# Performance work log

Measured on AMD Instinct MI355X. Metric: run time of the kernel, lower is better.

Reference implementation:

```python
import jax, jax.numpy as jnp
import numpy as np

B = 16384
QD = 2048   # query_dim
KD = 1024   # key_dim
HID = 1024  # hidden_dim = min(QD, KD)
NH = 16     # num_heads
HD = HID // NH  # head_dim = 64
LN_EPS = 1e-5


def _ln(x, w, b):
    m = jnp.mean(x, axis=-1, keepdims=True)
    v = jnp.mean((x - m) ** 2, axis=-1, keepdims=True)
    return (x - m) * jax.lax.rsqrt(v + LN_EPS) * w + b


def _lin(x, W, b):
    return x @ W.T + b


def setup_inputs() -> dict:
    key = jax.random.key(0)
    ks = jax.random.split(key, 12)
    p = lambda k, shape: jax.random.normal(k, shape, jnp.float32) * 0.02
    return dict(
        query_features=jax.random.normal(ks[0], (B, QD), jnp.float32),
        key_features=jax.random.normal(ks[1], (B, KD), jnp.float32),
        Wq=p(ks[2], (HID, QD)), bq=jnp.zeros((HID,), jnp.float32),
        ln_q_w=jnp.ones((HID,), jnp.float32), ln_q_b=jnp.zeros((HID,), jnp.float32),
        Wk=p(ks[3], (HID, KD)), bk=jnp.zeros((HID,), jnp.float32),
        ln_k_w=jnp.ones((HID,), jnp.float32), ln_k_b=jnp.zeros((HID,), jnp.float32),
        Wvq=p(ks[4], (HID, QD)), bvq=jnp.zeros((HID,), jnp.float32),
        Wvk=p(ks[5], (HID, KD)), bvk=jnp.zeros((HID,), jnp.float32),
        Wo=p(ks[6], (QD, HID)), bo=jnp.zeros((QD,), jnp.float32),
        ln_o_w=jnp.ones((QD,), jnp.float32), ln_o_b=jnp.zeros((QD,), jnp.float32),
        Wg1=p(ks[7], (HID, QD + KD)), bg1=jnp.zeros((HID,), jnp.float32),
        Wg2=p(ks[8], (1, HID)), bg2=jnp.zeros((1,), jnp.float32),
        Wc1=p(ks[9], (HID, QD + KD)), bc1=jnp.zeros((HID,), jnp.float32),
        Wc2=p(ks[10], (1, HID)), bc2=jnp.zeros((1,), jnp.float32),
    )


def reference(query_features, key_features,
              Wq, bq, ln_q_w, ln_q_b,
              Wk, bk, ln_k_w, ln_k_b,
              Wvq, bvq, Wvk, bvk,
              Wo, bo, ln_o_w, ln_o_b,
              Wg1, bg1, Wg2, bg2,
              Wc1, bc1, Wc2, bc2):
    b = query_features.shape[0]
    q = _ln(_lin(query_features, Wq, bq), ln_q_w, ln_q_b)      # [B, HID]
    k = _ln(_lin(key_features, Wk, bk), ln_k_w, ln_k_b)        # [B, HID]
    v_q = _lin(query_features, Wvq, bvq)  # computed in torch but unused
    v_k = _lin(key_features, Wvk, bvk)    # [B, HID]
    q = q.reshape(b, NH, HD)
    k = k.reshape(b, NH, HD)
    v_k = v_k.reshape(b, NH, HD)
    # NOTE: attention mixes over the HEAD axis (j == num_heads), per original einsum
    scores = jnp.einsum('bhd,bjd->bhj', q, k) / np.sqrt(HD).astype(np.float32)
    attn = jax.nn.softmax(scores, axis=-1)  # dropout p effectively 0 / eval mode
    attended = jnp.einsum('bhj,bjd->bhd', attn, v_k).reshape(b, HID)
    output = _ln(_lin(attended, Wo, bo), ln_o_w, ln_o_b)       # [B, QD]
    combined = jnp.concatenate([query_features, key_features], axis=1)  # [B, QD+KD]
    gate = jax.nn.sigmoid(_lin(jax.nn.gelu(_lin(combined, Wg1, bg1), approximate=False), Wg2, bg2))
    chem = jax.nn.sigmoid(_lin(jax.nn.gelu(_lin(combined, Wc1, bc1), approximate=False), Wc2, bc2))
    effective_gate = gate * chem  # [B, 1]
    return query_features + effective_gate * output
```

## Files before the change

kernel.cpp:

```cpp
#include <hip/hip_runtime.h>
#include <stdint.h>

#define QD 2048
#define KD 1024
#define HID 1024
#define NH 16
#define HD 64
#define CMBD 3072

typedef float  f32x4   __attribute__((ext_vector_type(4)));
typedef short  short8  __attribute__((ext_vector_type(8)));
typedef short  short4v __attribute__((ext_vector_type(4)));
typedef float  float4v __attribute__((ext_vector_type(4)));

__device__ inline float bf2f(short s) {
  unsigned u = ((unsigned)(unsigned short)s) << 16;
  return __builtin_bit_cast(float, u);
}
__device__ inline short f2bf(float f) {
  unsigned u = __builtin_bit_cast(unsigned, f);
  u = u + 0x7fff + ((u >> 16) & 1);
  return (short)(u >> 16);
}

__global__ void cvt_bf16(const float* __restrict__ s, short* __restrict__ d) {
  size_t i = ((size_t)blockIdx.x * blockDim.x + threadIdx.x) * 4;
  float4v v = *(const float4v*)(s + i);
  short4v o;
  o[0] = f2bf(v[0]); o[1] = f2bf(v[1]); o[2] = f2bf(v[2]); o[3] = f2bf(v[3]);
  *(short4v*)(d + i) = o;
}

__global__ void cvt_concat(const float* __restrict__ s, short* __restrict__ d,
                           int ncols4, int ldd) {
  int i = blockIdx.x * blockDim.x + threadIdx.x;
  int row = i / ncols4;
  int c4  = i - row * ncols4;
  float4v v = *(const float4v*)(s + (size_t)row * (ncols4 * 4) + c4 * 4);
  short4v o;
  o[0] = f2bf(v[0]); o[1] = f2bf(v[1]); o[2] = f2bf(v[2]); o[3] = f2bf(v[3]);
  *(short4v*)(d + (size_t)row * ldd + c4 * 4) = o;
}

#define EPI_NONE 0
#define EPI_GELU 1

typedef const __attribute__((address_space(1))) void gvoid_t;
typedef __attribute__((address_space(3))) void lvoid_t;

#define WAIT_VM(n)  asm volatile("s_waitcnt vmcnt(" #n ")" ::: "memory")
#define WAIT_LGKM0  asm volatile("s_waitcnt lgkmcnt(0)" ::: "memory")

template<int EPI>
__global__ __launch_bounds__(512, 2)
void gemm256(const short* __restrict__ A, size_t lda,
             const short* __restrict__ W,
             const float* __restrict__ bias,
             short* __restrict__ C, int N, int K) {
  extern __shared__ short ls[];
  const int tid  = threadIdx.x;
  const int lane = tid & 63;
  const int wave = tid >> 6;
  const int wm = wave >> 2, wn = wave & 3;
  const int fr = lane & 15, kq4 = lane >> 4;

  const int nwg = gridDim.x * gridDim.y;
  const int lin = blockIdx.y * gridDim.x + blockIdx.x;
  const int cpx = nwg >> 3;
  const int nid = (lin & 7) * cpx + (lin >> 3);
  const int bx = nid % gridDim.x, by = nid / gridDim.x;
  const size_t rowBase = (size_t)by * 256;
  const size_t colBase = (size_t)bx * 256;

  const int NT = K >> 5;

  f32x4 acc[8][4];
#pragma unroll
  for (int mi = 0; mi < 8; mi++)
#pragma unroll
    for (int ni = 0; ni < 4; ni++) acc[mi][ni] = (f32x4){0.f, 0.f, 0.f, 0.f};

  const int frsw = (kq4 ^ ((fr >> 1) & 3)) * 8;
  const int aoff = (wm * 128 + fr) * 32 + frsw;
  const int boff = 8192 + (wn * 64 + fr) * 32 + frsw;

  const int grow  = tid >> 2;
  const int slotx = (tid & 3) ^ ((tid >> 3) & 3);
  const short* pA0 = A + (rowBase + grow) * lda + slotx * 8;
  const short* pA1 = pA0 + (size_t)128 * lda;
  const short* pB0 = W + (colBase + grow) * (size_t)K + slotx * 8;
  const short* pB1 = pB0 + (size_t)128 * K;
  short* const dst0 = ls + tid * 8;

  auto STAGE = [&](int slot) {
    short* d = dst0 + slot * 16384;
    __builtin_amdgcn_global_load_lds((gvoid_t*)pA0, (lvoid_t*)d,            16, 0, 0);
    __builtin_amdgcn_global_load_lds((gvoid_t*)pA1, (lvoid_t*)(d + 4096),   16, 0, 0);
    __builtin_amdgcn_global_load_lds((gvoid_t*)pB0, (lvoid_t*)(d + 8192),   16, 0, 0);
    __builtin_amdgcn_global_load_lds((gvoid_t*)pB1, (lvoid_t*)(d + 12288),  16, 0, 0);
    pA0 += 32; pA1 += 32; pB0 += 32; pB1 += 32;
  };

  STAGE(0); STAGE(1); STAGE(2);
  WAIT_VM(8);
  __builtin_amdgcn_s_barrier();

  for (int t = 0; t < NT; ++t) {
    const short* sl = ls + (t & 3) * 16384;
    if (t + 3 < NT) STAGE((t + 3) & 3);

    short8 af[8], bf[4];
#pragma unroll
    for (int m = 0; m < 8; m++) af[m] = *(const short8*)(sl + aoff + m * 512);
#pragma unroll
    for (int n = 0; n < 4; n++) bf[n] = *(const short8*)(sl + boff + n * 512);

    __builtin_amdgcn_s_setprio(1);
#pragma unroll
    for (int m = 0; m < 8; m++)
#pragma unroll
      for (int n = 0; n < 4; n++)
        acc[m][n] = __builtin_amdgcn_mfma_f32_16x16x32_bf16(af[m], bf[n], acc[m][n], 0, 0, 0);
    __builtin_amdgcn_s_setprio(0);

    WAIT_LGKM0;
    const int rem = NT - 2 - t;
    if (rem >= 2)      { WAIT_VM(8); }
    else if (rem == 1) { WAIT_VM(4); }
    else               { WAIT_VM(0); }
    __builtin_amdgcn_s_barrier();
  }

#pragma unroll
  for (int mi = 0; mi < 8; mi++) {
    const size_t row0 = rowBase + wm * 128 + mi * 16 + kq4 * 4;
#pragma unroll
    for (int ni = 0; ni < 4; ni++) {
      const int col = (int)colBase + wn * 64 + ni * 16 + fr;
      const float bv = bias[col];
#pragma unroll
      for (int j = 0; j < 4; j++) {
        float x = acc[mi][ni][j] + bv;
        if (EPI == EPI_GELU) x = 0.5f * x * (1.f + erff(x * 0.70710678118f));
        C[(row0 + j) * (size_t)N + col] = f2bf(x);
      }
    }
  }
}

__device__ inline float2 block_sum2(float a, float b, float* sc) {
#pragma unroll
  for (int o = 32; o >= 1; o >>= 1) {
    a += __shfl_down(a, o);
    b += __shfl_down(b, o);
  }
  const int lane = threadIdx.x & 63, w = threadIdx.x >> 6;
  const int nw = blockDim.x >> 6;
  if (lane == 0) { sc[w * 2] = a; sc[w * 2 + 1] = b; }
  __syncthreads();
  float ra = 0.f, rb = 0.f;
  for (int i = 0; i < nw; i++) { ra += sc[i * 2]; rb += sc[i * 2 + 1]; }
  __syncthreads();
  return make_float2(ra, rb);
}

__global__ __launch_bounds__(256)
void attn_ln(const short* __restrict__ qp, const short* __restrict__ kv,
             const float* __restrict__ lnqw, const float* __restrict__ lnqb,
             const float* __restrict__ lnkw, const float* __restrict__ lnkb,
             short* __restrict__ att) {
  __shared__ float qs[HID];
  __shared__ float ks[NH * 65];
  __shared__ float vs[HID];
  __shared__ float aw[256];
  __shared__ float red[8];
  const int t = threadIdx.x;
  const size_t row = blockIdx.x;

  short4v q4 = *(const short4v*)(qp + row * HID + t * 4);
  short4v k4 = *(const short4v*)(kv + row * 2048 + t * 4);
  short4v v4 = *(const short4v*)(kv + row * 2048 + 1024 + t * 4);
  float qv[4], kvv[4];
  float sq = 0.f, sqq = 0.f, sk = 0.f, skk = 0.f;
#pragma unroll
  for (int i = 0; i < 4; i++) {
    qv[i] = bf2f(q4[i]); sq += qv[i]; sqq += qv[i] * qv[i];
    kvv[i] = bf2f(k4[i]); sk += kvv[i]; skk += kvv[i] * kvv[i];
  }
  float2 rq = block_sum2(sq, sqq, red);
  float mq = rq.x / HID, vq = rq.y / HID - mq * mq;
  float rsq = rsqrtf(vq + 1e-5f);
  float2 rk = block_sum2(sk, skk, red);
  float mk = rk.x / HID, vv = rk.y / HID - mk * mk;
  float rsk = rsqrtf(vv + 1e-5f);
#pragma unroll
  for (int i = 0; i < 4; i++) {
    const int idx = t * 4 + i;
    qs[idx] = (qv[i] - mq) * rsq * lnqw[idx] + lnqb[idx];
    ks[(idx >> 6) * 65 + (idx & 63)] = (kvv[i] - mk) * rsk * lnkw[idx] + lnkb[idx];
    vs[idx] = bf2f(v4[i]);
  }
  __syncthreads();

  const int h = t >> 4, j = t & 15;
  float s = 0.f;
#pragma unroll 8
  for (int d = 0; d < 64; d++) s += qs[h * 64 + d] * ks[j * 65 + d];
  s *= 0.125f;
  float mx = s;
#pragma unroll
  for (int o = 8; o >= 1; o >>= 1) mx = fmaxf(mx, __shfl_xor(mx, o, 16));
  float e = __expf(s - mx);
  float sum = e;
#pragma unroll
  for (int o = 8; o >= 1; o >>= 1) sum += __shfl_xor(sum, o, 16);
  aw[t] = e / sum;
  __syncthreads();

  const int dB = (t & 15) * 4;
  float o0 = 0.f, o1 = 0.f, o2 = 0.f, o3 = 0.f;
#pragma unroll
  for (int jj = 0; jj < 16; jj++) {
    const float w = aw[h * 16 + jj];
    const float* vp = &vs[jj * 64 + dB];
    o0 += w * vp[0]; o1 += w * vp[1]; o2 += w * vp[2]; o3 += w * vp[3];
  }
  short4v o4;
  o4[0] = f2bf(o0); o4[1] = f2bf(o1); o4[2] = f2bf(o2); o4[3] = f2bf(o3);
  *(short4v*)(att + row * HID + h * 64 + dB) = o4;
}

__global__ __launch_bounds__(256)
void gate_kernel(const short* __restrict__ hgc,
                 const float* __restrict__ wg2, const float* __restrict__ bg2,
                 const float* __restrict__ wc2, const float* __restrict__ bc2,
                 float* __restrict__ eg) {
  __shared__ float red[8];
  const int t = threadIdx.x;
  const size_t row = blockIdx.x;
  short4v g4 = *(const short4v*)(hgc + row * 2048 + t * 4);
  short4v c4 = *(const short4v*)(hgc + row * 2048 + 1024 + t * 4);
  float sg = 0.f, sc = 0.f;
#pragma unroll
  for (int i = 0; i < 4; i++) {
    sg += bf2f(g4[i]) * wg2[t * 4 + i];
    sc += bf2f(c4[i]) * wc2[t * 4 + i];
  }
  float2 r = block_sum2(sg, sc, red);
  if (t == 0) {
    float g = 1.f / (1.f + __expf(-(r.x + bg2[0])));
    float c = 1.f / (1.f + __expf(-(r.y + bc2[0])));
    eg[row] = g * c;
  }
}

__global__ __launch_bounds__(256)
void final_kernel(const short* __restrict__ opre, const float* __restrict__ qf,
                  const float* __restrict__ eg,
                  const float* __restrict__ lnow, const float* __restrict__ lnob,
                  float* __restrict__ out) {
  __shared__ float red[8];
  const int t = threadIdx.x;
  const size_t row = blockIdx.x;
  short8 o8 = *(const short8*)(opre + row * QD + t * 8);
  float x[8];
  float s = 0.f, ss = 0.f;
#pragma unroll
  for (int i = 0; i < 8; i++) { x[i] = bf2f(o8[i]); s += x[i]; ss += x[i] * x[i]; }
  float2 r = block_sum2(s, ss, red);
  float m = r.x / QD, v = r.y / QD - m * m;
  float rs = rsqrtf(v + 1e-5f);
  float g = eg[row];
  float4v oa, ob;
#pragma unroll
  for (int i = 0; i < 8; i++) {
    const int c = t * 8 + i;
    float y = (x[i] - m) * rs * lnow[c] + lnob[c];
    float r2 = qf[row * QD + c] + g * y;
    if (i < 4) oa[i] = r2; else ob[i - 4] = r2;
  }
  *(float4v*)(out + row * QD + t * 8) = oa;
  *(float4v*)(out + row * QD + t * 8 + 4) = ob;
}

extern "C" void kernel_launch(void* const* d_in, const int* in_sizes, int n_in,
                              void* d_out, int out_size, void* d_ws, size_t ws_size,
                              hipStream_t stream) {
  const float* qf   = (const float*)d_in[0];
  const float* kf   = (const float*)d_in[1];
  const float* Wq   = (const float*)d_in[2];
  const float* bq   = (const float*)d_in[3];
  const float* lnqw = (const float*)d_in[4];
  const float* lnqb = (const float*)d_in[5];
  const float* Wk   = (const float*)d_in[6];
  const float* bk   = (const float*)d_in[7];
  const float* lnkw = (const float*)d_in[8];
  const float* lnkb = (const float*)d_in[9];
  const float* Wvk  = (const float*)d_in[12];
  const float* bvk  = (const float*)d_in[13];
  const float* Wo   = (const float*)d_in[14];
  const float* bo   = (const float*)d_in[15];
  const float* lnow = (const float*)d_in[16];
  const float* lnob = (const float*)d_in[17];
  const float* Wg1  = (const float*)d_in[18];
  const float* bg1  = (const float*)d_in[19];
  const float* Wg2  = (const float*)d_in[20];
  const float* bg2  = (const float*)d_in[21];
  const float* Wc1  = (const float*)d_in[22];
  const float* bc1  = (const float*)d_in[23];
  const float* Wc2  = (const float*)d_in[24];
  const float* bc2  = (const float*)d_in[25];

  const int rows = in_sizes[0] / QD;

  char* ws = (char*)d_ws;
  size_t off = 0;
  auto alloc = [&](size_t bytes) -> char* {
    char* p = ws + off;
    off += (bytes + 255) & ~(size_t)255;
    return p;
  };
  short* cmb  = (short*)alloc((size_t)rows * CMBD * 2);
  short* wqb  = (short*)alloc((size_t)HID * QD * 2);
  short* wkv  = (short*)alloc((size_t)2 * HID * KD * 2);
  short* wob  = (short*)alloc((size_t)QD * HID * 2);
  short* wgc  = (short*)alloc((size_t)2 * HID * CMBD * 2);
  short* hgc  = (short*)alloc((size_t)rows * 2048 * 2);
  short* qp   = (short*)alloc((size_t)rows * HID * 2);
  short* kvp  = (short*)alloc((size_t)rows * 2048 * 2);
  float* eg   = (float*)alloc((size_t)rows * 4);
  float* bgc  = (float*)alloc(2048 * 4);
  float* bkv  = (float*)alloc(2048 * 4);
  short* att  = hgc;
  short* opre = cmb;

  hipMemcpyAsync(bgc, bg1, HID * 4, hipMemcpyDeviceToDevice, stream);
  hipMemcpyAsync(bgc + HID, bc1, HID * 4, hipMemcpyDeviceToDevice, stream);
  hipMemcpyAsync(bkv, bk, HID * 4, hipMemcpyDeviceToDevice, stream);
  hipMemcpyAsync(bkv + HID, bvk, HID * 4, hipMemcpyDeviceToDevice, stream);

  cvt_concat<<<rows * 2, 256, 0, stream>>>(qf, cmb, QD / 4, CMBD);
  cvt_concat<<<rows, 256, 0, stream>>>(kf, cmb + QD, KD / 4, CMBD);
  cvt_bf16<<<(HID * QD / 4) / 256, 256, 0, stream>>>(Wq, wqb);
  cvt_bf16<<<(HID * KD / 4) / 256, 256, 0, stream>>>(Wk, wkv);
  cvt_bf16<<<(HID * KD / 4) / 256, 256, 0, stream>>>(Wvk, wkv + (size_t)HID * KD);
  cvt_bf16<<<(QD * HID / 4) / 256, 256, 0, stream>>>(Wo, wob);
  cvt_bf16<<<(HID * CMBD / 4) / 256, 256, 0, stream>>>(Wg1, wgc);
  cvt_bf16<<<(HID * CMBD / 4) / 256, 256, 0, stream>>>(Wc1, wgc + (size_t)HID * CMBD);

  hipFuncSetAttribute((const void*)gemm256<EPI_GELU>,
                      hipFuncAttributeMaxDynamicSharedMemorySize, 131072);
  hipFuncSetAttribute((const void*)gemm256<EPI_NONE>,
                      hipFuncAttributeMaxDynamicSharedMemorySize, 131072);

  const dim3 blk(512);
  const int mt = rows / 256;
  const size_t lds = 131072;

  gemm256<EPI_GELU><<<dim3(2048 / 256, mt), blk, lds, stream>>>(cmb, CMBD, wgc, bgc, hgc, 2048, CMBD);
  gate_kernel<<<rows, 256, 0, stream>>>(hgc, Wg2, bg2, Wc2, bc2, eg);
  gemm256<EPI_NONE><<<dim3(1024 / 256, mt), blk, lds, stream>>>(cmb, CMBD, wqb, bq, qp, 1024, QD);
  gemm256<EPI_NONE><<<dim3(2048 / 256, mt), blk, lds, stream>>>(cmb + QD, CMBD, wkv, bkv, kvp, 2048, KD);
  attn_ln<<<rows, 256, 0, stream>>>(qp, kvp, lnqw, lnqb, lnkw, lnkb, att);
  gemm256<EPI_NONE><<<dim3(2048 / 256, mt), blk, lds, stream>>>(att, HID, wob, bo, opre, 2048, HID);
  final_kernel<<<rows, 256, 0, stream>>>(opre, qf, eg, lnow, lnob, (float*)d_out);
}
```

Before: 656.0 us.

## Load GEMM weight fragments straight to registers and shrink LDS staging to three A buffers

The GEMM kernel no longer stages the weight (B) tile through LDS. Each wave loads its own B fragments from global memory into double-buffered registers, and only the A tile goes through a 3-slot LDS ring held in a static 48KB shared array. This removes LDS traffic and capacity pressure for B, which may allow more blocks per CU. In exchange, B fragments are fetched per wave with less coalescing and are reloaded redundantly by waves sharing a column, and the loop now needs two barriers per iteration.

```diff
diff --git a/kernel.cpp b/kernel.cpp
--- a/kernel.cpp
+++ b/kernel.cpp
@@ -49,7 +49,6 @@
 typedef __attribute__((address_space(3))) void lvoid_t;
 
 #define WAIT_VM(n)  asm volatile("s_waitcnt vmcnt(" #n ")" ::: "memory")
-#define WAIT_LGKM0  asm volatile("s_waitcnt lgkmcnt(0)" ::: "memory")
 
 template<int EPI>
 __global__ __launch_bounds__(512, 2)
@@ -57,7 +56,7 @@
              const short* __restrict__ W,
              const float* __restrict__ bias,
              short* __restrict__ C, int N, int K) {
-  extern __shared__ short ls[];
+  __shared__ short ls[3 * 8192];
   const int tid  = threadIdx.x;
   const int lane = tid & 63;
   const int wave = tid >> 6;
@@ -82,54 +81,62 @@
 
   const int frsw = (kq4 ^ ((fr >> 1) & 3)) * 8;
   const int aoff = (wm * 128 + fr) * 32 + frsw;
-  const int boff = 8192 + (wn * 64 + fr) * 32 + frsw;
 
   const int grow  = tid >> 2;
   const int slotx = (tid & 3) ^ ((tid >> 3) & 3);
   const short* pA0 = A + (rowBase + grow) * lda + slotx * 8;
   const short* pA1 = pA0 + (size_t)128 * lda;
-  const short* pB0 = W + (colBase + grow) * (size_t)K + slotx * 8;
-  const short* pB1 = pB0 + (size_t)128 * K;
   short* const dst0 = ls + tid * 8;
 
   auto STAGE = [&](int slot) {
-    short* d = dst0 + slot * 16384;
-    __builtin_amdgcn_global_load_lds((gvoid_t*)pA0, (lvoid_t*)d,            16, 0, 0);
-    __builtin_amdgcn_global_load_lds((gvoid_t*)pA1, (lvoid_t*)(d + 4096),   16, 0, 0);
-    __builtin_amdgcn_global_load_lds((gvoid_t*)pB0, (lvoid_t*)(d + 8192),   16, 0, 0);
-    __builtin_amdgcn_global_load_lds((gvoid_t*)pB1, (lvoid_t*)(d + 12288),  16, 0, 0);
-    pA0 += 32; pA1 += 32; pB0 += 32; pB1 += 32;
+    short* d = dst0 + slot * 8192;
+    __builtin_amdgcn_global_load_lds((gvoid_t*)pA0, (lvoid_t*)d,          16, 0, 0);
+    __builtin_amdgcn_global_load_lds((gvoid_t*)pA1, (lvoid_t*)(d + 4096), 16, 0, 0);
+    pA0 += 32; pA1 += 32;
   };
 
-  STAGE(0); STAGE(1); STAGE(2);
-  WAIT_VM(8);
-  __builtin_amdgcn_s_barrier();
-
-  for (int t = 0; t < NT; ++t) {
-    const short* sl = ls + (t & 3) * 16384;
-    if (t + 3 < NT) STAGE((t + 3) & 3);
-
-    short8 af[8], bf[4];
-#pragma unroll
-    for (int m = 0; m < 8; m++) af[m] = *(const short8*)(sl + aoff + m * 512);
-#pragma unroll
-    for (int n = 0; n < 4; n++) bf[n] = *(const short8*)(sl + boff + n * 512);
-
-    __builtin_amdgcn_s_setprio(1);
-#pragma unroll
-    for (int m = 0; m < 8; m++)
-#pragma unroll
-      for (int n = 0; n < 4; n++)
-        acc[m][n] = __builtin_amdgcn_mfma_f32_16x16x32_bf16(af[m], bf[n], acc[m][n], 0, 0, 0);
-    __builtin_amdgcn_s_setprio(0);
-
-    WAIT_LGKM0;
-    const int rem = NT - 2 - t;
-    if (rem >= 2)      { WAIT_VM(8); }
-    else if (rem == 1) { WAIT_VM(4); }
-    else               { WAIT_VM(0); }
-    __builtin_amdgcn_s_barrier();
-  }
+  const short* pb = W + (colBase + wn * 64 + fr) * (size_t)K + kq4 * 8;
+  short8 bE[4], bO[4];
+
+  STAGE(0);
+#pragma unroll
+  for (int n = 0; n < 4; n++) bE[n] = *(const short8*)(pb + n * 16 * (size_t)K);
+  pb += 32;
+  STAGE(1);
+
+#define GITER(T, bC, bN)                                                      \
+  {                                                                           \
+    const int t_ = (T);                                                       \
+    if (t_ + 1 < NT) {                                                        \
+      _Pragma("unroll")                                                       \
+      for (int n = 0; n < 4; n++)                                             \
+        bN[n] = *(const short8*)(pb + n * 16 * (size_t)K);                    \
+      pb += 32;                                                               \
+    }                                                                         \
+    if (t_ + 2 < NT) STAGE((t_ + 2) % 3);                                     \
+    if (t_ + 2 < NT)       { WAIT_VM(12); }                                   \
+    else if (t_ + 2 == NT) { WAIT_VM(10); }                                   \
+    else                   { WAIT_VM(4); }                                    \
+    __builtin_amdgcn_s_barrier();                                             \
+    const short* sl_ = ls + (t_ % 3) * 8192;                                  \
+    short8 af_[8];                                                            \
+    _Pragma("unroll")                                                         \
+    for (int m = 0; m < 8; m++) af_[m] = *(const short8*)(sl_ + aoff + m * 512); \
+    __builtin_amdgcn_s_setprio(1);                                            \
+    _Pragma("unroll")                                                         \
+    for (int m = 0; m < 8; m++)                                               \
+      _Pragma("unroll")                                                       \
+      for (int n = 0; n < 4; n++)                                             \
+        acc[m][n] = __builtin_amdgcn_mfma_f32_16x16x32_bf16(af_[m], bC[n], acc[m][n], 0, 0, 0); \
+    __builtin_amdgcn_s_setprio(0);                                            \
+    __builtin_amdgcn_s_barrier();                                             \
+  }
+
+  for (int t = 0; t < NT; t += 2) {
+    GITER(t,     bE, bO)
+    GITER(t + 1, bO, bE)
+  }
+#undef GITER
 
 #pragma unroll
   for (int mi = 0; mi < 8; mi++) {
@@ -348,20 +355,14 @@
   cvt_bf16<<<(HID * CMBD / 4) / 256, 256, 0, stream>>>(Wg1, wgc);
   cvt_bf16<<<(HID * CMBD / 4) / 256, 256, 0, stream>>>(Wc1, wgc + (size_t)HID * CMBD);
 
-  hipFuncSetAttribute((const void*)gemm256<EPI_GELU>,
-                      hipFuncAttributeMaxDynamicSharedMemorySize, 131072);
-  hipFuncSetAttribute((const void*)gemm256<EPI_NONE>,
-                      hipFuncAttributeMaxDynamicSharedMemorySize, 131072);
-
   const dim3 blk(512);
   const int mt = rows / 256;
-  const size_t lds = 131072;
-
-  gemm256<EPI_GELU><<<dim3(2048 / 256, mt), blk, lds, stream>>>(cmb, CMBD, wgc, bgc, hgc, 2048, CMBD);
+
+  gemm256<EPI_GELU><<<dim3(2048 / 256, mt), blk, 0, stream>>>(cmb, CMBD, wgc, bgc, hgc, 2048, CMBD);
   gate_kernel<<<rows, 256, 0, stream>>>(hgc, Wg2, bg2, Wc2, bc2, eg);
-  gemm256<EPI_NONE><<<dim3(1024 / 256, mt), blk, lds, stream>>>(cmb, CMBD, wqb, bq, qp, 1024, QD);
-  gemm256<EPI_NONE><<<dim3(2048 / 256, mt), blk, lds, stream>>>(cmb + QD, CMBD, wkv, bkv, kvp, 2048, KD);
+  gemm256<EPI_NONE><<<dim3(1024 / 256, mt), blk, 0, stream>>>(cmb, CMBD, wqb, bq, qp, 1024, QD);
+  gemm256<EPI_NONE><<<dim3(2048 / 256, mt), blk, 0, stream>>>(cmb + QD, CMBD, wkv, bkv, kvp, 2048, KD);
   attn_ln<<<rows, 256, 0, stream>>>(qp, kvp, lnqw, lnqb, lnkw, lnkb, att);
-  gemm256<EPI_NONE><<<dim3(2048 / 256, mt), blk, lds, stream>>>(att, HID, wob, bo, opre, 2048, HID);
+  gemm256<EPI_NONE><<<dim3(2048 / 256, mt), blk, 0, stream>>>(att, HID, wob, bo, opre, 2048, HID);
   final_kernel<<<rows, 256, 0, stream>>>(opre, qf, eg, lnow, lnob, (float*)d_out);
 }
```

Measured after the change: 886.9 us. 35.2% more time.

## Fuse gate second layer into GEMM epilogue and retile GEMM to four waves

Applied to the files above, without the earlier changes.

The gate/chem second linear layer (GELU then dot with Wg2/Wc2) now runs in the first GEMM's epilogue, with per-row partial sums accumulated by atomicAdd. This removes the hidden-activation store, the separate gate kernel and its re-read. The sigmoid product moves into the final kernel. The GEMM also changes from 512 threads with 4-deep dynamic LDS buffering to 256 threads, each wave holding a 128x128 accumulator, with 3-deep static LDS buffering. This raises register pressure and lowers wave count per CU, and the atomics make the gate sums nondeterministic. The attention LN reductions are merged into a single block reduction.

```diff
diff --git a/kernel.cpp b/kernel.cpp
--- a/kernel.cpp
+++ b/kernel.cpp
@@ -44,24 +44,27 @@
 
 #define EPI_NONE 0
 #define EPI_GELU 1
+#define EPI_GATE 2
 
 typedef const __attribute__((address_space(1))) void gvoid_t;
 typedef __attribute__((address_space(3))) void lvoid_t;
 
 #define WAIT_VM(n)  asm volatile("s_waitcnt vmcnt(" #n ")" ::: "memory")
-#define WAIT_LGKM0  asm volatile("s_waitcnt lgkmcnt(0)" ::: "memory")
+
+#define SLOT 16384
 
 template<int EPI>
-__global__ __launch_bounds__(512, 2)
+__global__ __launch_bounds__(256, 1)
 void gemm256(const short* __restrict__ A, size_t lda,
              const short* __restrict__ W,
              const float* __restrict__ bias,
-             short* __restrict__ C, int N, int K) {
-  extern __shared__ short ls[];
+             short* __restrict__ C, int N, int K,
+             const float* __restrict__ w2, float* __restrict__ egp, int rowsTot) {
+  __shared__ short ls[3 * SLOT];
   const int tid  = threadIdx.x;
   const int lane = tid & 63;
   const int wave = tid >> 6;
-  const int wm = wave >> 2, wn = wave & 3;
+  const int wm = wave >> 1, wn = wave & 1;
   const int fr = lane & 15, kq4 = lane >> 4;
 
   const int nwg = gridDim.x * gridDim.y;
@@ -74,92 +77,134 @@
 
   const int NT = K >> 5;
 
-  f32x4 acc[8][4];
+  f32x4 acc[8][8];
 #pragma unroll
   for (int mi = 0; mi < 8; mi++)
 #pragma unroll
-    for (int ni = 0; ni < 4; ni++) acc[mi][ni] = (f32x4){0.f, 0.f, 0.f, 0.f};
+    for (int ni = 0; ni < 8; ni++) acc[mi][ni] = (f32x4){0.f, 0.f, 0.f, 0.f};
 
   const int frsw = (kq4 ^ ((fr >> 1) & 3)) * 8;
   const int aoff = (wm * 128 + fr) * 32 + frsw;
-  const int boff = 8192 + (wn * 64 + fr) * 32 + frsw;
+  const int boff = 8192 + (wn * 128 + fr) * 32 + frsw;
 
   const int grow  = tid >> 2;
   const int slotx = (tid & 3) ^ ((tid >> 3) & 3);
-  const short* pA0 = A + (rowBase + grow) * lda + slotx * 8;
-  const short* pA1 = pA0 + (size_t)128 * lda;
-  const short* pB0 = W + (colBase + grow) * (size_t)K + slotx * 8;
-  const short* pB1 = pB0 + (size_t)128 * K;
+  const short* pA = A + (rowBase + grow) * lda + slotx * 8;
+  const short* pB = W + (colBase + grow) * (size_t)K + slotx * 8;
+  const size_t stepA = 64 * lda, stepB = 64 * (size_t)K;
   short* const dst0 = ls + tid * 8;
 
   auto STAGE = [&](int slot) {
-    short* d = dst0 + slot * 16384;
-    __builtin_amdgcn_global_load_lds((gvoid_t*)pA0, (lvoid_t*)d,            16, 0, 0);
-    __builtin_amdgcn_global_load_lds((gvoid_t*)pA1, (lvoid_t*)(d + 4096),   16, 0, 0);
-    __builtin_amdgcn_global_load_lds((gvoid_t*)pB0, (lvoid_t*)(d + 8192),   16, 0, 0);
-    __builtin_amdgcn_global_load_lds((gvoid_t*)pB1, (lvoid_t*)(d + 12288),  16, 0, 0);
-    pA0 += 32; pA1 += 32; pB0 += 32; pB1 += 32;
+    short* d = dst0 + slot * SLOT;
+#pragma unroll
+    for (int p = 0; p < 4; p++)
+      __builtin_amdgcn_global_load_lds((gvoid_t*)(pA + p * stepA),
+          (lvoid_t*)(d + p * 2048), 16, 0, 0);
+#pragma unroll
+    for (int p = 0; p < 4; p++)
+      __builtin_amdgcn_global_load_lds((gvoid_t*)(pB + p * stepB),
+          (lvoid_t*)(d + 8192 + p * 2048), 16, 0, 0);
+    pA += 32; pB += 32;
   };
 
-  STAGE(0); STAGE(1); STAGE(2);
+  STAGE(0); STAGE(1);
   WAIT_VM(8);
   __builtin_amdgcn_s_barrier();
 
   for (int t = 0; t < NT; ++t) {
-    const short* sl = ls + (t & 3) * 16384;
-    if (t + 3 < NT) STAGE((t + 3) & 3);
-
-    short8 af[8], bf[4];
+    if (t + 2 < NT) STAGE((t + 2) % 3);
+    const short* sl = ls + (t % 3) * SLOT;
+    short8 af[8], bf[8];
 #pragma unroll
     for (int m = 0; m < 8; m++) af[m] = *(const short8*)(sl + aoff + m * 512);
 #pragma unroll
-    for (int n = 0; n < 4; n++) bf[n] = *(const short8*)(sl + boff + n * 512);
+    for (int n = 0; n < 8; n++) bf[n] = *(const short8*)(sl + boff + n * 512);
 
     __builtin_amdgcn_s_setprio(1);
 #pragma unroll
     for (int m = 0; m < 8; m++)
 #pragma unroll
-      for (int n = 0; n < 4; n++)
+      for (int n = 0; n < 8; n++)
         acc[m][n] = __builtin_amdgcn_mfma_f32_16x16x32_bf16(af[m], bf[n], acc[m][n], 0, 0, 0);
     __builtin_amdgcn_s_setprio(0);
 
-    WAIT_LGKM0;
-    const int rem = NT - 2 - t;
-    if (rem >= 2)      { WAIT_VM(8); }
-    else if (rem == 1) { WAIT_VM(4); }
-    else               { WAIT_VM(0); }
+    if (t + 2 < NT) { WAIT_VM(8); }
+    else            { WAIT_VM(0); }
     __builtin_amdgcn_s_barrier();
   }
 
-#pragma unroll
-  for (int mi = 0; mi < 8; mi++) {
-    const size_t row0 = rowBase + wm * 128 + mi * 16 + kq4 * 4;
-#pragma unroll
-    for (int ni = 0; ni < 4; ni++) {
-      const int col = (int)colBase + wn * 64 + ni * 16 + fr;
-      const float bv = bias[col];
+  if (EPI == EPI_GATE) {
+    float w2v[8], bvv[8];
+#pragma unroll
+    for (int ni = 0; ni < 8; ni++) {
+      const int c = (int)colBase + wn * 128 + ni * 16 + fr;
+      w2v[ni] = w2[c]; bvv[ni] = bias[c];
+    }
+    const int half = (colBase >= 1024) ? 1 : 0;
+#pragma unroll
+    for (int mi = 0; mi < 8; mi++) {
+      float sj[4] = {0.f, 0.f, 0.f, 0.f};
+#pragma unroll
+      for (int ni = 0; ni < 8; ni++)
+#pragma unroll
+        for (int j = 0; j < 4; j++) {
+          float x = acc[mi][ni][j] + bvv[ni];
+          float g = 0.5f * x * (1.f + erff(x * 0.70710678118f));
+          sj[j] += g * w2v[ni];
+        }
 #pragma unroll
       for (int j = 0; j < 4; j++) {
-        float x = acc[mi][ni][j] + bv;
-        if (EPI == EPI_GELU) x = 0.5f * x * (1.f + erff(x * 0.70710678118f));
-        C[(row0 + j) * (size_t)N + col] = f2bf(x);
+#pragma unroll
+        for (int o = 8; o >= 1; o >>= 1) sj[j] += __shfl_xor(sj[j], o);
+        if (fr == 0) {
+          const int row = (int)rowBase + wm * 128 + mi * 16 + kq4 * 4 + j;
+          atomicAdd(egp + half * rowsTot + row, sj[j]);
+        }
       }
     }
-  }
-}
-
-__device__ inline float2 block_sum2(float a, float b, float* sc) {
+  } else {
+#pragma unroll
+    for (int mi = 0; mi < 8; mi++) {
+      const size_t row0 = rowBase + wm * 128 + mi * 16 + kq4 * 4;
+#pragma unroll
+      for (int ni = 0; ni < 8; ni++) {
+        const int col = (int)colBase + wn * 128 + ni * 16 + fr;
+        const float bv = bias[col];
+#pragma unroll
+        for (int j = 0; j < 4; j++) {
+          float x = acc[mi][ni][j] + bv;
+          if (EPI == EPI_GELU) x = 0.5f * x * (1.f + erff(x * 0.70710678118f));
+          C[(row0 + j) * (size_t)N + col] = f2bf(x);
+        }
+      }
+    }
+  }
+}
+
+__device__ inline float4 block_sum4(float a, float b, float c, float d, float* sc) {
 #pragma unroll
   for (int o = 32; o >= 1; o >>= 1) {
-    a += __shfl_down(a, o);
-    b += __shfl_down(b, o);
+    a += __shfl_down(a, o); b += __shfl_down(b, o);
+    c += __shfl_down(c, o); d += __shfl_down(d, o);
   }
   const int lane = threadIdx.x & 63, w = threadIdx.x >> 6;
   const int nw = blockDim.x >> 6;
-  if (lane == 0) { sc[w * 2] = a; sc[w * 2 + 1] = b; }
+  if (lane == 0) { sc[w*4] = a; sc[w*4+1] = b; sc[w*4+2] = c; sc[w*4+3] = d; }
+  __syncthreads();
+  float ra = 0.f, rb = 0.f, rc = 0.f, rd = 0.f;
+  for (int i = 0; i < nw; i++) { ra += sc[i*4]; rb += sc[i*4+1]; rc += sc[i*4+2]; rd += sc[i*4+3]; }
+  __syncthreads();
+  return make_float4(ra, rb, rc, rd);
+}
+__device__ inline float2 block_sum2(float a, float b, float* sc) {
+#pragma unroll
+  for (int o = 32; o >= 1; o >>= 1) { a += __shfl_down(a, o); b += __shfl_down(b, o); }
+  const int lane = threadIdx.x & 63, w = threadIdx.x >> 6;
+  const int nw = blockDim.x >> 6;
+  if (lane == 0) { sc[w*2] = a; sc[w*2+1] = b; }
   __syncthreads();
   float ra = 0.f, rb = 0.f;
-  for (int i = 0; i < nw; i++) { ra += sc[i * 2]; rb += sc[i * 2 + 1]; }
+  for (int i = 0; i < nw; i++) { ra += sc[i*2]; rb += sc[i*2+1]; }
   __syncthreads();
   return make_float2(ra, rb);
 }
@@ -173,7 +218,7 @@
   __shared__ float ks[NH * 65];
   __shared__ float vs[HID];
   __shared__ float aw[256];
-  __shared__ float red[8];
+  __shared__ float red[16];
   const int t = threadIdx.x;
   const size_t row = blockIdx.x;
 
@@ -187,11 +232,10 @@
     qv[i] = bf2f(q4[i]); sq += qv[i]; sqq += qv[i] * qv[i];
     kvv[i] = bf2f(k4[i]); sk += kvv[i]; skk += kvv[i] * kvv[i];
   }
-  float2 rq = block_sum2(sq, sqq, red);
-  float mq = rq.x / HID, vq = rq.y / HID - mq * mq;
+  float4 r4 = block_sum4(sq, sqq, sk, skk, red);
+  float mq = r4.x / HID, vq = r4.y / HID - mq * mq;
   float rsq = rsqrtf(vq + 1e-5f);
-  float2 rk = block_sum2(sk, skk, red);
-  float mk = rk.x / HID, vv = rk.y / HID - mk * mk;
+  float mk = r4.z / HID, vv = r4.w / HID - mk * mk;
   float rsk = rsqrtf(vv + 1e-5f);
 #pragma unroll
   for (int i = 0; i < 4; i++) {
@@ -231,32 +275,9 @@
 }
 
 __global__ __launch_bounds__(256)
-void gate_kernel(const short* __restrict__ hgc,
-                 const float* __restrict__ wg2, const float* __restrict__ bg2,
-                 const float* __restrict__ wc2, const float* __restrict__ bc2,
-                 float* __restrict__ eg) {
-  __shared__ float red[8];
-  const int t = threadIdx.x;
-  const size_t row = blockIdx.x;
-  short4v g4 = *(const short4v*)(hgc + row * 2048 + t * 4);
-  short4v c4 = *(const short4v*)(hgc + row * 2048 + 1024 + t * 4);
-  float sg = 0.f, sc = 0.f;
-#pragma unroll
-  for (int i = 0; i < 4; i++) {
-    sg += bf2f(g4[i]) * wg2[t * 4 + i];
-    sc += bf2f(c4[i]) * wc2[t * 4 + i];
-  }
-  float2 r = block_sum2(sg, sc, red);
-  if (t == 0) {
-    float g = 1.f / (1.f + __expf(-(r.x + bg2[0])));
-    float c = 1.f / (1.f + __expf(-(r.y + bc2[0])));
-    eg[row] = g * c;
-  }
-}
-
-__global__ __launch_bounds__(256)
 void final_kernel(const short* __restrict__ opre, const float* __restrict__ qf,
-                  const float* __restrict__ eg,
+                  const float* __restrict__ egp, int rowsTot,
+                  const float* __restrict__ bg2, const float* __restrict__ bc2,
                   const float* __restrict__ lnow, const float* __restrict__ lnob,
                   float* __restrict__ out) {
   __shared__ float red[8];
@@ -270,7 +291,9 @@
   float2 r = block_sum2(s, ss, red);
   float m = r.x / QD, v = r.y / QD - m * m;
   float rs = rsqrtf(v + 1e-5f);
-  float g = eg[row];
+  float gg = 1.f / (1.f + __expf(-(egp[row] + bg2[0])));
+  float gc = 1.f / (1.f + __expf(-(egp[rowsTot + row] + bc2[0])));
+  float g = gg * gc;
   float4v oa, ob;
 #pragma unroll
   for (int i = 0; i < 8; i++) {
@@ -328,9 +351,10 @@
   short* hgc  = (short*)alloc((size_t)rows * 2048 * 2);
   short* qp   = (short*)alloc((size_t)rows * HID * 2);
   short* kvp  = (short*)alloc((size_t)rows * 2048 * 2);
-  float* eg   = (float*)alloc((size_t)rows * 4);
+  float* egp  = (float*)alloc((size_t)2 * rows * 4);
   float* bgc  = (float*)alloc(2048 * 4);
   float* bkv  = (float*)alloc(2048 * 4);
+  float* w2gc = (float*)alloc(2048 * 4);
   short* att  = hgc;
   short* opre = cmb;
 
@@ -338,6 +362,9 @@
   hipMemcpyAsync(bgc + HID, bc1, HID * 4, hipMemcpyDeviceToDevice, stream);
   hipMemcpyAsync(bkv, bk, HID * 4, hipMemcpyDeviceToDevice, stream);
   hipMemcpyAsync(bkv + HID, bvk, HID * 4, hipMemcpyDeviceToDevice, stream);
+  hipMemcpyAsync(w2gc, Wg2, HID * 4, hipMemcpyDeviceToDevice, stream);
+  hipMemcpyAsync(w2gc + HID, Wc2, HID * 4, hipMemcpyDeviceToDevice, stream);
+  hipMemsetAsync(egp, 0, (size_t)2 * rows * 4, stream);
 
   cvt_concat<<<rows * 2, 256, 0, stream>>>(qf, cmb, QD / 4, CMBD);
   cvt_concat<<<rows, 256, 0, stream>>>(kf, cmb + QD, KD / 4, CMBD);
@@ -348,20 +375,13 @@
   cvt_bf16<<<(HID * CMBD / 4) / 256, 256, 0, stream>>>(Wg1, wgc);
   cvt_bf16<<<(HID * CMBD / 4) / 256, 256, 0, stream>>>(Wc1, wgc + (size_t)HID * CMBD);
 
-  hipFuncSetAttribute((const void*)gemm256<EPI_GELU>,
-                      hipFuncAttributeMaxDynamicSharedMemorySize, 131072);
-  hipFuncSetAttribute((const void*)gemm256<EPI_NONE>,
-                      hipFuncAttributeMaxDynamicSharedMemorySize, 131072);
-
-  const dim3 blk(512);
+  const dim3 blk(256);
   const int mt = rows / 256;
-  const size_t lds = 131072;
-
-  gemm256<EPI_GELU><<<dim3(2048 / 256, mt), blk, lds, stream>>>(cmb, CMBD, wgc, bgc, hgc, 2048, CMBD);
-  gate_kernel<<<rows, 256, 0, stream>>>(hgc, Wg2, bg2, Wc2, bc2, eg);
-  gemm256<EPI_NONE><<<dim3(1024 / 256, mt), blk, lds, stream>>>(cmb, CMBD, wqb, bq, qp, 1024, QD);
-  gemm256<EPI_NONE><<<dim3(2048 / 256, mt), blk, lds, stream>>>(cmb + QD, CMBD, wkv, bkv, kvp, 2048, KD);
+
+  gemm256<EPI_GATE><<<dim3(2048 / 256, mt), blk, 0, stream>>>(cmb, CMBD, wgc, bgc, hgc, 2048, CMBD, w2gc, egp, rows);
+  gemm256<EPI_NONE><<<dim3(1024 / 256, mt), blk, 0, stream>>>(cmb, CMBD, wqb, bq, qp, 1024, QD, nullptr, nullptr, 0);
+  gemm256<EPI_NONE><<<dim3(2048 / 256, mt), blk, 0, stream>>>(cmb + QD, CMBD, wkv, bkv, kvp, 2048, KD, nullptr, nullptr, 0);
   attn_ln<<<rows, 256, 0, stream>>>(qp, kvp, lnqw, lnqb, lnkw, lnkb, att);
-  gemm256<EPI_NONE><<<dim3(2048 / 256, mt), blk, lds, stream>>>(att, HID, wob, bo, opre, 2048, HID);
-  final_kernel<<<rows, 256, 0, stream>>>(opre, qf, eg, lnow, lnob, (float*)d_out);
-}
+  gemm256<EPI_NONE><<<dim3(2048 / 256, mt), blk, 0, stream>>>(att, HID, wob, bo, opre, 2048, HID, nullptr, nullptr, 0);
+  final_kernel<<<rows, 256, 0, stream>>>(opre, qf, egp, rows, bg2, bc2, lnow, lnob, (float*)d_out);
+}
```

Result: slower. 704.5 us (+7.4%).
